# Kernel optimization log

Measured on AMD Instinct MI355X. Metric: run time of the kernel, lower is better.

## Reference

```python
import jax, jax.numpy as jnp
import numpy as np

B, S, D_IN, D_MID, D_OUT, V = 32, 512, 768, 128, 4, 100000
N = B * S  # static upper bound on number of unique (vocab_id, batch_id) pairs


def setup_inputs() -> dict:
    key = jax.random.key(0)
    k1, k2, k3, k4 = jax.random.split(key, 4)
    vocab_ids = jax.random.randint(k1, (B, S), 0, V)
    embeddings = jax.random.normal(k2, (B, S, D_IN), jnp.float32)
    # nn.Linear default init (kaiming-uniform-ish); exact distribution is irrelevant for correctness
    lin_bound = 1.0 / np.sqrt(D_IN)
    W1 = jax.random.uniform(k3, (D_IN, D_MID), jnp.float32, -lin_bound, lin_bound)
    b1 = jnp.zeros((D_MID,), jnp.float32)
    # kaiming_uniform_(a=sqrt(5)) on (V, D_MID, D_OUT): fan_in = D_MID*D_OUT, bound = 1/sqrt(fan_in)
    enc_bound = 1.0 / np.sqrt(D_MID * D_OUT)
    encoder_weights = jax.random.uniform(k4, (V, D_MID, D_OUT), jnp.float32, -enc_bound, enc_bound)
    return {"vocab_ids": vocab_ids, "embeddings": embeddings, "W1": W1, "b1": b1,
            "encoder_weights": encoder_weights}


def reference(vocab_ids, embeddings, W1, b1, encoder_weights):
    # Composite key = vocab_id * B + batch_id -> same lexicographic (vocab, batch) order
    # as torch.unique(dim=0) on stacked (vocab_id, batch_id) pairs.
    batch_ids = jnp.arange(B, dtype=vocab_ids.dtype)[:, None]            # (B,1)
    keys = (vocab_ids * B + batch_ids).reshape(-1)                        # (N,)
    # Static-size unique for jit; padded slots (fill) receive zero-sum embeddings.
    uniq_keys, inv = jnp.unique(keys, size=N, fill_value=0, return_inverse=True)
    flat_emb = embeddings.reshape(N, D_IN)
    summed = jax.ops.segment_sum(flat_emb, inv.reshape(-1), num_segments=N)  # (N, D_IN)
    h = jnp.tanh(summed @ W1 + b1)                                        # (N, D_MID)
    uniq_vocab = uniq_keys // B
    uniq_batch = uniq_keys % B
    Wtok = encoder_weights[uniq_vocab]                                    # (N, D_MID, D_OUT) gather
    encoded = jax.nn.sigmoid(jnp.einsum('bi,bio->bo', h, Wtok))           # (N, D_OUT)
    ids = jnp.stack([uniq_vocab, uniq_batch], axis=1)                     # (N, 2)
    return ids, encoded
```

## Files before the change

### kernel.cpp

```cpp
#include <hip/hip_runtime.h>
#include <hip/hip_bf16.h>

#define NELEM 16384
#define DIN 768
#define DMID 128
#define DOUT 4

typedef __attribute__((ext_vector_type(8))) short short8;
typedef __attribute__((ext_vector_type(4))) float f32x4;

__device__ __forceinline__ unsigned f2bf(float f) {
    unsigned u = __float_as_uint(f);
    return (u + 0x7FFFu + ((u >> 16) & 1u)) >> 16;
}


#define FAST_WS 557384
#define SORT_BLOCKS 64

__device__ __forceinline__ void gsync(unsigned* bar) {
    __syncthreads();
    if (threadIdx.x == 0) {
        unsigned g = __hip_atomic_load(&bar[1], __ATOMIC_ACQUIRE, __HIP_MEMORY_SCOPE_AGENT);
        unsigned a = __hip_atomic_fetch_add(&bar[0], 1u, __ATOMIC_ACQ_REL, __HIP_MEMORY_SCOPE_AGENT);
        if (a + 1u == (unsigned)SORT_BLOCKS) {
            __hip_atomic_store(&bar[0], 0u, __ATOMIC_RELAXED, __HIP_MEMORY_SCOPE_AGENT);
            __hip_atomic_store(&bar[1], g + 1u, __ATOMIC_RELEASE, __HIP_MEMORY_SCOPE_AGENT);
        } else {
            while (__hip_atomic_load(&bar[1], __ATOMIC_ACQUIRE, __HIP_MEMORY_SCOPE_AGENT) == g) {
                __builtin_amdgcn_s_sleep(2);
            }
        }
    }
    __syncthreads();
}

__global__ __launch_bounds__(256) void prep_kernel(
    const int* __restrict__ vocab_ids, const float* __restrict__ W1,
    unsigned* __restrict__ P0, unsigned* __restrict__ hist0,
    unsigned* __restrict__ histZ, unsigned short* __restrict__ WtG,
    unsigned* __restrict__ bar) {
    const int t = threadIdx.x;
    const int bx = blockIdx.x;
    if (bx < 64) {
        __shared__ unsigned h[256];
        h[t] = 0;
        int e = bx * 256 + t;
        unsigned word = ((unsigned)vocab_ids[e] << 14) | (unsigned)e;
        P0[e] = word;
        __syncthreads();
        atomicAdd(&h[(word >> 9) & 255u], 1u);
        __syncthreads();
        hist0[t * 64 + bx] = h[t];
        histZ[bx * 512 + t] = 0;
        histZ[bx * 512 + 256 + t] = 0;
        if (bx == 0 && t == 0) bar[0] = 0;
    } else {
        int idx = (bx - 64) * 256 + t;
        int c = idx / DIN;
        int k = idx - c * DIN;
        WtG[idx] = (unsigned short)f2bf(W1[k * DMID + c]);
    }
}

template <bool HASNEXT>
__device__ __forceinline__ void scatter_pass(
    const unsigned* __restrict__ src, unsigned* __restrict__ dst,
    const unsigned* __restrict__ histCur, unsigned* __restrict__ histNext,
    int shift, int nshift, int blk, int t,
    unsigned* base_lds, unsigned* whist, unsigned* wsum) {
    const int lane = t & 63;
    const int w = t >> 6;

    unsigned x = src[blk * 256 + t];
    unsigned d = (x >> shift) & 255u;

    whist[t] = 0; whist[256 + t] = 0; whist[512 + t] = 0; whist[768 + t] = 0;

    unsigned rowsum = 0, myprefix = 0;
    const uint4* row = (const uint4*)(histCur + t * 64);
#pragma unroll
    for (int q = 0; q < 16; ++q) {
        uint4 h4 = row[q];
        int b = q * 4;
        rowsum += h4.x + h4.y + h4.z + h4.w;
        if (b + 0 < blk) myprefix += h4.x;
        if (b + 1 < blk) myprefix += h4.y;
        if (b + 2 < blk) myprefix += h4.z;
        if (b + 3 < blk) myprefix += h4.w;
    }
    unsigned inc = rowsum;
#pragma unroll
    for (int off = 1; off < 64; off <<= 1) {
        unsigned y = __shfl_up(inc, off);
        if (lane >= off) inc += y;
    }
    if (lane == 63) wsum[w] = inc;
    __syncthreads();
    unsigned wo = 0;
    for (int w2 = 0; w2 < w; ++w2) wo += wsum[w2];
    base_lds[t] = wo + (inc - rowsum) + myprefix;

    unsigned long long m = ~0ull;
#pragma unroll
    for (int bit = 0; bit < 8; ++bit) {
        unsigned long long bb = __ballot((d >> bit) & 1u);
        m &= ((d >> bit) & 1u) ? bb : ~bb;
    }
    int inrank = __popcll(m & ((1ull << lane) - 1ull));
    if (inrank == 0) whist[w * 256 + d] = (unsigned)__popcll(m);
    __syncthreads();
    unsigned cross = 0;
    for (int w2 = 0; w2 < w; ++w2) cross += whist[w2 * 256 + d];
    unsigned dstpos = base_lds[d] + cross + (unsigned)inrank;
    dst[dstpos] = x;
    if (HASNEXT) {
        unsigned dn = (x >> nshift) & 255u;
        atomicAdd(&histNext[dn * 64 + (dstpos >> 8)], 1u);
    }
}

__global__ __launch_bounds__(256) void coop_sort_kernel(
    unsigned* __restrict__ P0, unsigned* __restrict__ P1,
    const unsigned* __restrict__ hist0, unsigned* __restrict__ hist1,
    unsigned* __restrict__ hist2,
    unsigned short* __restrict__ RS, float* __restrict__ out_ids,
    unsigned* __restrict__ bar) {
    __shared__ unsigned base_lds[256];
    __shared__ unsigned whist[4 * 256];
    __shared__ unsigned wsum[4];
    const int t = threadIdx.x;
    const int blk = blockIdx.x;
    unsigned* gsum = bar + 2;

    scatter_pass<true >(P0, P1, hist0, hist1, 9, 17, blk, t, base_lds, whist, wsum);
    gsync(bar);
    scatter_pass<true >(P1, P0, hist1, hist2, 17, 25, blk, t, base_lds, whist, wsum);
    gsync(bar);
    scatter_pass<false>(P0, P1, hist2, nullptr, 25, 0, blk, t, base_lds, whist, wsum);
    gsync(bar);

    const int e = blk * 256 + t;
    const int lane = t & 63;
    const int w = t >> 6;
    unsigned word = P1[e];
    unsigned key = word >> 9;
    bool f = (e == 0) || ((P1[e - 1] >> 9) != key);
    unsigned long long bb = __ballot(f ? 1 : 0);
    unsigned lrank = (unsigned)__popcll(bb & ((1ull << lane) - 1ull));
    if (lane == 0) wsum[w] = (unsigned)__popcll(bb);
    __syncthreads();
    unsigned woff = 0, btot = 0;
#pragma unroll
    for (int w2 = 0; w2 < 4; ++w2) {
        if (w2 < w) woff += wsum[w2];
        btot += wsum[w2];
    }
    if (t == 0) gsum[blk] = btot;
    gsync(bar);
    unsigned prefix = 0, U = 0;
#pragma unroll
    for (int b = 0; b < 64; ++b) {
        unsigned g = gsum[b];
        if (b < blk) prefix += g;
        U += g;
    }
    if (f) {
        unsigned r = prefix + woff + lrank;
        RS[r] = (unsigned short)e;
        out_ids[2 * r + 0] = (float)(word >> 14);
        out_ids[2 * r + 1] = (float)(key & 31u);
    }
    if ((unsigned)e >= U) {
        RS[e] = (unsigned short)NELEM;
        out_ids[2 * e + 0] = 0.0f;
        out_ids[2 * e + 1] = 0.0f;
    }
    if (e == 0) RS[NELEM] = (unsigned short)NELEM;
}

#define SORT_SMEM (65536 + 65536 + 4096 + 64)

__global__ __launch_bounds__(1024) void sort_transpose_kernel(
    const int* __restrict__ vocab_ids,
    const float* __restrict__ W1,
    unsigned int* __restrict__ G,
    unsigned short* __restrict__ RS,
    unsigned short* __restrict__ WtG,
    float* __restrict__ out_ids) {
    const int t = threadIdx.x;
    if (blockIdx.x != 0) {
        int idx = (blockIdx.x - 1) * 1024 + t;
        if (idx < DMID * DIN) {
            int c = idx / DIN;
            int k = idx - c * DIN;
            WtG[idx] = (unsigned short)f2bf(W1[k * DMID + c]);
        }
        return;
    }
    extern __shared__ char smem[];
    unsigned* Gs     = (unsigned*)smem;
    unsigned* histDM = (unsigned*)(smem + 65536);
    unsigned* sums   = (unsigned*)(smem + 131072);
    unsigned* totalU = (unsigned*)(smem + 135168);

    for (int e = t; e < NELEM; e += 1024)
        Gs[e] = ((unsigned)vocab_ids[e] << 14) | (unsigned)e;
    __syncthreads();

    for (int pass = 0; pass < 6; ++pass) {
        const int shift = 9 + pass * 4;
        unsigned v[16];
#pragma unroll
        for (int i = 0; i < 16; ++i) v[i] = Gs[t * 16 + i];
#pragma unroll
        for (int d = 0; d < 16; ++d) histDM[d * 1024 + t] = 0;
#pragma unroll
        for (int i = 0; i < 16; ++i) histDM[((v[i] >> shift) & 15u) * 1024 + t] += 1;
        __syncthreads();
        unsigned lex[16]; unsigned run = 0;
#pragma unroll
        for (int i = 0; i < 16; ++i) { unsigned x = histDM[t * 16 + i]; lex[i] = run; run += x; }
        sums[t] = run;
        __syncthreads();
        if (t < 64) {
            unsigned s[16]; unsigned tot = 0;
#pragma unroll
            for (int i = 0; i < 16; ++i) { unsigned x = sums[t * 16 + i]; s[i] = tot; tot += x; }
            unsigned incv = tot;
#pragma unroll
            for (int off = 1; off < 64; off <<= 1) {
                unsigned y = __shfl_up(incv, off);
                if (t >= off) incv += y;
            }
            unsigned excl = incv - tot;
#pragma unroll
            for (int i = 0; i < 16; ++i) sums[t * 16 + i] = excl + s[i];
        }
        __syncthreads();
#pragma unroll
        for (int i = 0; i < 16; ++i) histDM[t * 16 + i] = sums[t] + lex[i];
        __syncthreads();
        unsigned mycnt[16];
#pragma unroll
        for (int d = 0; d < 16; ++d) mycnt[d] = histDM[d * 1024 + t];
#pragma unroll
        for (int i = 0; i < 16; ++i) {
            unsigned d = (v[i] >> shift) & 15u;
            Gs[mycnt[d]++] = v[i];
        }
        __syncthreads();
    }

    unsigned v[16];
#pragma unroll
    for (int i = 0; i < 16; ++i) v[i] = Gs[t * 16 + i];
    unsigned pk = (t == 0) ? 0xFFFFFFFFu : (Gs[t * 16 - 1] >> 9);
    unsigned fm = 0;
#pragma unroll
    for (int i = 0; i < 16; ++i) {
        unsigned key = v[i] >> 9;
        if (key != pk) fm |= (1u << i);
        pk = key;
    }
    sums[t] = (unsigned)__popc(fm);
    __syncthreads();
    if (t < 64) {
        unsigned s[16]; unsigned tot = 0;
#pragma unroll
        for (int i = 0; i < 16; ++i) { unsigned x = sums[t * 16 + i]; s[i] = tot; tot += x; }
        unsigned incv = tot;
#pragma unroll
        for (int off = 1; off < 64; off <<= 1) {
            unsigned y = __shfl_up(incv, off);
            if (t >= off) incv += y;
        }
        unsigned excl = incv - tot;
#pragma unroll
        for (int i = 0; i < 16; ++i) sums[t * 16 + i] = excl + s[i];
        if (t == 63) *totalU = incv;
    }
    __syncthreads();
    unsigned r = sums[t];
#pragma unroll
    for (int i = 0; i < 16; ++i) {
        if (fm & (1u << i)) {
            RS[r] = (unsigned short)(t * 16 + i);
            out_ids[2 * r + 0] = (float)(v[i] >> 14);
            out_ids[2 * r + 1] = (float)((v[i] >> 9) & 31u);
            ++r;
        }
    }
    const unsigned U = *totalU;
    for (int u = t; u < NELEM; u += 1024) {
        if ((unsigned)u >= U) {
            RS[u] = (unsigned short)NELEM;
            out_ids[2 * u + 0] = 0.0f;
            out_ids[2 * u + 1] = 0.0f;
        }
        G[u] = Gs[u];
    }
    if (t == 0) RS[NELEM] = (unsigned short)NELEM;
}

#define FBM 16
__global__ __launch_bounds__(256) void fused_kernel(
    const unsigned* __restrict__ G,
    const unsigned short* __restrict__ RS,
    const unsigned short* __restrict__ WtG,
    const float* __restrict__ emb,
    const float* __restrict__ b1,
    const float* __restrict__ enc,
    float* __restrict__ out_enc) {
    __shared__ char smem[20736];

    const int t = threadIdx.x;
    const int u0 = blockIdx.x * FBM;
    const int l = t & 63;
    const int w = t >> 6;

    const int ar = t >> 4;
    const int ak4 = t & 15;
    const int rs_a = (int)RS[u0 + ar];
    const int re_a = (int)RS[u0 + ar + 1];

    f32x4 acc0 = {0.f, 0.f, 0.f, 0.f};
    f32x4 acc1 = {0.f, 0.f, 0.f, 0.f};

    for (int kk = 0; kk < DIN; kk += 64) {
        __syncthreads();
        {
            float s0 = 0.f, s1 = 0.f, s2 = 0.f, s3 = 0.f;
            const float* base = emb + (size_t)(kk + ak4 * 4);
            for (int p = rs_a; p < re_a; ++p) {
                unsigned idx = G[p] & 16383u;
                const float4 e4 = *(const float4*)(base + (size_t)idx * DIN);
                s0 += e4.x; s1 += e4.y; s2 += e4.z; s3 += e4.w;
            }
            uint2 packed;
            packed.x = f2bf(s0) | (f2bf(s1) << 16);
            packed.y = f2bf(s2) | (f2bf(s3) << 16);
            *(uint2*)(smem + ar * 144 + ak4 * 8) = packed;
        }
        {
#pragma unroll
            for (int i = 0; i < 4; ++i) {
                int q = t + i * 256;
                int c = q >> 3;
                int uo = q & 7;
                uint4 dv = *(const uint4*)(WtG + (size_t)c * DIN + kk + uo * 8);
                *(uint4*)(smem + 2304 + c * 144 + uo * 16) = dv;
            }
        }
        __syncthreads();
        {
            const int arow = l & 15;
            const int ull = l >> 4;
#pragma unroll
            for (int kf = 0; kf < 2; ++kf) {
                short8 aF = *(const short8*)(smem + arow * 144 + kf * 64 + ull * 16);
                short8 bF0 = *(const short8*)(smem + 2304 + (w * 32 + arow) * 144 + kf * 64 + ull * 16);
                short8 bF1 = *(const short8*)(smem + 2304 + (w * 32 + 16 + arow) * 144 + kf * 64 + ull * 16);
                acc0 = __builtin_amdgcn_mfma_f32_16x16x32_bf16(aF, bF0, acc0, 0, 0, 0);
                acc1 = __builtin_amdgcn_mfma_f32_16x16x32_bf16(aF, bF1, acc1, 0, 0, 0);
            }
        }
    }
    __syncthreads();
    {
        float* Hs = (float*)smem;
        const int col0 = w * 32 + (l & 15);
        const int rbase = (l >> 4) * 4;
#pragma unroll
        for (int reg = 0; reg < 4; ++reg) {
            Hs[(rbase + reg) * 132 + col0] = tanhf(acc0[reg] + b1[col0]);
            Hs[(rbase + reg) * 132 + col0 + 16] = tanhf(acc1[reg] + b1[col0 + 16]);
        }
    }
    __syncthreads();
    {
        const float* Hs = (const float*)smem;
        const int r = t >> 4;
        const int g = t & 15;
        const int u = u0 + r;
        const int rs = (int)RS[u];
        const int re = (int)RS[u + 1];
        unsigned vocab = (rs < re) ? (G[rs] >> 14) : 0u;
        const float4* wrow = (const float4*)(enc + (size_t)vocab * (DMID * DOUT));
        float ax = 0.f, ay = 0.f, az = 0.f, aw = 0.f;
#pragma unroll
        for (int jj = 0; jj < 8; ++jj) {
            int j = jj * 16 + g;
            float4 w4 = wrow[j];
            float hv = Hs[r * 132 + j];
            ax += hv * w4.x; ay += hv * w4.y; az += hv * w4.z; aw += hv * w4.w;
        }
#pragma unroll
        for (int off = 1; off < 16; off <<= 1) {
            ax += __shfl_xor(ax, off);
            ay += __shfl_xor(ay, off);
            az += __shfl_xor(az, off);
            aw += __shfl_xor(aw, off);
        }
        if (g == 0) {
            float4 o;
            o.x = 1.f / (1.f + expf(-ax));
            o.y = 1.f / (1.f + expf(-ay));
            o.z = 1.f / (1.f + expf(-az));
            o.w = 1.f / (1.f + expf(-aw));
            *(float4*)(out_enc + (size_t)u * 4) = o;
        }
    }
}

extern "C" void kernel_launch(void* const* d_in, const int* in_sizes, int n_in,
                              void* d_out, int out_size, void* d_ws, size_t ws_size,
                              hipStream_t stream) {
    const int*   vocab_ids = (const int*)d_in[0];
    const float* emb       = (const float*)d_in[1];
    const float* W1        = (const float*)d_in[2];
    const float* b1        = (const float*)d_in[3];
    const float* enc       = (const float*)d_in[4];
    float* out = (float*)d_out;

    float* out_ids = out;
    float* out_enc = out + NELEM * 2;

    char* ws = (char*)d_ws;

    if (ws_size >= FAST_WS) {
        unsigned*       P0    = (unsigned*)(ws + 0);
        unsigned*       P1    = (unsigned*)(ws + 65536);
        unsigned*       hist0 = (unsigned*)(ws + 131072);
        unsigned*       hist1 = (unsigned*)(ws + 196608);
        unsigned*       hist2 = (unsigned*)(ws + 262144);
        unsigned short* RS    = (unsigned short*)(ws + 327680);
        unsigned short* WtG   = (unsigned short*)(ws + 360512);
        unsigned*       bar   = (unsigned*)(ws + 557120);

        prep_kernel<<<448, 256, 0, stream>>>(vocab_ids, W1, P0, hist0, hist1, WtG, bar);
        coop_sort_kernel<<<SORT_BLOCKS, 256, 0, stream>>>(P0, P1, hist0, hist1, hist2,
                                                          RS, out_ids, bar);
        fused_kernel<<<NELEM / FBM, 256, 0, stream>>>(P1, RS, WtG, emb, b1, enc, out_enc);
    } else {
        unsigned int*   G   = (unsigned int*)(ws);
        unsigned short* RS  = (unsigned short*)(ws + 65536);
        unsigned short* WtG = (unsigned short*)(ws + 98432);

        hipFuncSetAttribute((const void*)sort_transpose_kernel,
                            hipFuncAttributeMaxDynamicSharedMemorySize, SORT_SMEM);
        sort_transpose_kernel<<<1 + 96, 1024, SORT_SMEM, stream>>>(
            vocab_ids, W1, G, RS, WtG, out_ids);
        fused_kernel<<<NELEM / FBM, 256, 0, stream>>>(G, RS, WtG, emb, b1, enc, out_enc);
    }
}
```

Before: 71.79 us.

## Fold prep into cooperative sort kernel with monotonic-counter grid barriers

Merges the histogram/transposition prep kernel into the persistent sort kernel, adding a grid barrier after prep. It replaces the generation-based barrier with a monotonically increasing counter reset by a memset each launch, and uses relaxed agent-scope atomics for cross-block data. Histogram layout is changed to block-major so each pass reads per-digit counts coalesced across threads. This removes one kernel launch but adds a memset, and the W1 transpose now runs on only 64 blocks.

```diff
diff --git a/kernel.cpp b/kernel.cpp
--- a/kernel.cpp
+++ b/kernel.cpp
@@ -15,52 +15,28 @@
 }
 
 
-#define FAST_WS 557384
-#define SORT_BLOCKS 64
-
-__device__ __forceinline__ void gsync(unsigned* bar) {
+#define FAST_WS 557440
+#define SB 64
+
+__device__ __forceinline__ unsigned aload(const unsigned* p) {
+    return __hip_atomic_load((unsigned*)p, __ATOMIC_RELAXED, __HIP_MEMORY_SCOPE_AGENT);
+}
+__device__ __forceinline__ void astore(unsigned* p, unsigned v) {
+    __hip_atomic_store(p, v, __ATOMIC_RELAXED, __HIP_MEMORY_SCOPE_AGENT);
+}
+__device__ __forceinline__ void aadd(unsigned* p, unsigned v) {
+    __hip_atomic_fetch_add(p, v, __ATOMIC_RELAXED, __HIP_MEMORY_SCOPE_AGENT);
+}
+
+__device__ __forceinline__ void gbar(unsigned* cnt, unsigned thresh) {
     __syncthreads();
     if (threadIdx.x == 0) {
-        unsigned g = __hip_atomic_load(&bar[1], __ATOMIC_ACQUIRE, __HIP_MEMORY_SCOPE_AGENT);
-        unsigned a = __hip_atomic_fetch_add(&bar[0], 1u, __ATOMIC_ACQ_REL, __HIP_MEMORY_SCOPE_AGENT);
-        if (a + 1u == (unsigned)SORT_BLOCKS) {
-            __hip_atomic_store(&bar[0], 0u, __ATOMIC_RELAXED, __HIP_MEMORY_SCOPE_AGENT);
-            __hip_atomic_store(&bar[1], g + 1u, __ATOMIC_RELEASE, __HIP_MEMORY_SCOPE_AGENT);
-        } else {
-            while (__hip_atomic_load(&bar[1], __ATOMIC_ACQUIRE, __HIP_MEMORY_SCOPE_AGENT) == g) {
-                __builtin_amdgcn_s_sleep(2);
-            }
-        }
-    }
-    __syncthreads();
-}
-
-__global__ __launch_bounds__(256) void prep_kernel(
-    const int* __restrict__ vocab_ids, const float* __restrict__ W1,
-    unsigned* __restrict__ P0, unsigned* __restrict__ hist0,
-    unsigned* __restrict__ histZ, unsigned short* __restrict__ WtG,
-    unsigned* __restrict__ bar) {
-    const int t = threadIdx.x;
-    const int bx = blockIdx.x;
-    if (bx < 64) {
-        __shared__ unsigned h[256];
-        h[t] = 0;
-        int e = bx * 256 + t;
-        unsigned word = ((unsigned)vocab_ids[e] << 14) | (unsigned)e;
-        P0[e] = word;
-        __syncthreads();
-        atomicAdd(&h[(word >> 9) & 255u], 1u);
-        __syncthreads();
-        hist0[t * 64 + bx] = h[t];
-        histZ[bx * 512 + t] = 0;
-        histZ[bx * 512 + 256 + t] = 0;
-        if (bx == 0 && t == 0) bar[0] = 0;
-    } else {
-        int idx = (bx - 64) * 256 + t;
-        int c = idx / DIN;
-        int k = idx - c * DIN;
-        WtG[idx] = (unsigned short)f2bf(W1[k * DMID + c]);
-    }
+        __hip_atomic_fetch_add(cnt, 1u, __ATOMIC_ACQ_REL, __HIP_MEMORY_SCOPE_AGENT);
+        while (__hip_atomic_load(cnt, __ATOMIC_RELAXED, __HIP_MEMORY_SCOPE_AGENT) < thresh)
+            __builtin_amdgcn_s_sleep(1);
+        (void)__hip_atomic_load(cnt, __ATOMIC_ACQUIRE, __HIP_MEMORY_SCOPE_AGENT);
+    }
+    __syncthreads();
 }
 
 template <bool HASNEXT>
@@ -72,22 +48,17 @@
     const int lane = t & 63;
     const int w = t >> 6;
 
-    unsigned x = src[blk * 256 + t];
+    unsigned x = aload(&src[blk * 256 + t]);
     unsigned d = (x >> shift) & 255u;
 
     whist[t] = 0; whist[256 + t] = 0; whist[512 + t] = 0; whist[768 + t] = 0;
 
     unsigned rowsum = 0, myprefix = 0;
-    const uint4* row = (const uint4*)(histCur + t * 64);
-#pragma unroll
-    for (int q = 0; q < 16; ++q) {
-        uint4 h4 = row[q];
-        int b = q * 4;
-        rowsum += h4.x + h4.y + h4.z + h4.w;
-        if (b + 0 < blk) myprefix += h4.x;
-        if (b + 1 < blk) myprefix += h4.y;
-        if (b + 2 < blk) myprefix += h4.z;
-        if (b + 3 < blk) myprefix += h4.w;
+#pragma unroll
+    for (int b = 0; b < SB; ++b) {
+        unsigned h = aload(&histCur[b * 256 + t]);
+        rowsum += h;
+        if (b < blk) myprefix += h;
     }
     unsigned inc = rowsum;
 #pragma unroll
@@ -113,70 +84,97 @@
     unsigned cross = 0;
     for (int w2 = 0; w2 < w; ++w2) cross += whist[w2 * 256 + d];
     unsigned dstpos = base_lds[d] + cross + (unsigned)inrank;
-    dst[dstpos] = x;
+    astore(&dst[dstpos], x);
     if (HASNEXT) {
         unsigned dn = (x >> nshift) & 255u;
-        atomicAdd(&histNext[dn * 64 + (dstpos >> 8)], 1u);
-    }
-}
-
-__global__ __launch_bounds__(256) void coop_sort_kernel(
+        aadd(&histNext[(dstpos >> 8) * 256 + dn], 1u);
+    }
+    __syncthreads();
+}
+
+__global__ __launch_bounds__(256) void sort_mega_kernel(
+    const int* __restrict__ vocab_ids, const float* __restrict__ W1,
     unsigned* __restrict__ P0, unsigned* __restrict__ P1,
-    const unsigned* __restrict__ hist0, unsigned* __restrict__ hist1,
+    unsigned* __restrict__ hist0, unsigned* __restrict__ hist1,
     unsigned* __restrict__ hist2,
-    unsigned short* __restrict__ RS, float* __restrict__ out_ids,
-    unsigned* __restrict__ bar) {
+    unsigned short* __restrict__ RS, unsigned short* __restrict__ WtG,
+    float* __restrict__ out_ids,
+    unsigned* __restrict__ bar, unsigned* __restrict__ gsum) {
     __shared__ unsigned base_lds[256];
     __shared__ unsigned whist[4 * 256];
     __shared__ unsigned wsum[4];
     const int t = threadIdx.x;
     const int blk = blockIdx.x;
-    unsigned* gsum = bar + 2;
+
+    const int e = blk * 256 + t;
+    {
+        whist[t] = 0;
+        unsigned word = ((unsigned)vocab_ids[e] << 14) | (unsigned)e;
+        astore(&P0[e], word);
+        __syncthreads();
+        atomicAdd(&whist[(word >> 9) & 255u], 1u);
+        __syncthreads();
+        astore(&hist0[blk * 256 + t], whist[t]);
+        astore(&hist1[blk * 256 + t], 0u);
+        astore(&hist2[blk * 256 + t], 0u);
+#pragma unroll
+        for (int i = 0; i < 6; ++i) {
+            int j = blk * 1536 + i * 256 + t;
+            int k = j >> 7;
+            int c = j & 127;
+            WtG[c * DIN + k] = (unsigned short)f2bf(W1[j]);
+        }
+        __syncthreads();
+    }
+    gbar(bar, SB * 1);
 
     scatter_pass<true >(P0, P1, hist0, hist1, 9, 17, blk, t, base_lds, whist, wsum);
-    gsync(bar);
+    gbar(bar, SB * 2);
     scatter_pass<true >(P1, P0, hist1, hist2, 17, 25, blk, t, base_lds, whist, wsum);
-    gsync(bar);
+    gbar(bar, SB * 3);
     scatter_pass<false>(P0, P1, hist2, nullptr, 25, 0, blk, t, base_lds, whist, wsum);
-    gsync(bar);
-
-    const int e = blk * 256 + t;
-    const int lane = t & 63;
-    const int w = t >> 6;
-    unsigned word = P1[e];
+    gbar(bar, SB * 4);
+
+    unsigned word = aload(&P1[e]);
     unsigned key = word >> 9;
-    bool f = (e == 0) || ((P1[e - 1] >> 9) != key);
-    unsigned long long bb = __ballot(f ? 1 : 0);
-    unsigned lrank = (unsigned)__popcll(bb & ((1ull << lane) - 1ull));
-    if (lane == 0) wsum[w] = (unsigned)__popcll(bb);
-    __syncthreads();
-    unsigned woff = 0, btot = 0;
-#pragma unroll
-    for (int w2 = 0; w2 < 4; ++w2) {
-        if (w2 < w) woff += wsum[w2];
-        btot += wsum[w2];
-    }
-    if (t == 0) gsum[blk] = btot;
-    gsync(bar);
-    unsigned prefix = 0, U = 0;
-#pragma unroll
-    for (int b = 0; b < 64; ++b) {
-        unsigned g = gsum[b];
-        if (b < blk) prefix += g;
-        U += g;
-    }
-    if (f) {
-        unsigned r = prefix + woff + lrank;
-        RS[r] = (unsigned short)e;
-        out_ids[2 * r + 0] = (float)(word >> 14);
-        out_ids[2 * r + 1] = (float)(key & 31u);
-    }
-    if ((unsigned)e >= U) {
-        RS[e] = (unsigned short)NELEM;
-        out_ids[2 * e + 0] = 0.0f;
-        out_ids[2 * e + 1] = 0.0f;
-    }
-    if (e == 0) RS[NELEM] = (unsigned short)NELEM;
+    bool f = (e == 0) || ((aload(&P1[e - 1]) >> 9) != key);
+    {
+        const int lane = t & 63;
+        const int w = t >> 6;
+        unsigned long long bb = __ballot(f ? 1 : 0);
+        unsigned lrank = (unsigned)__popcll(bb & ((1ull << lane) - 1ull));
+        if (lane == 0) wsum[w] = (unsigned)__popcll(bb);
+        __syncthreads();
+        unsigned woff = 0, btot = 0;
+#pragma unroll
+        for (int w2 = 0; w2 < 4; ++w2) {
+            if (w2 < w) woff += wsum[w2];
+            btot += wsum[w2];
+        }
+        if (t == 0) astore(&gsum[blk], btot);
+        gbar(bar, SB * 5);
+        if (t < SB) base_lds[t] = aload(&gsum[t]);
+        __syncthreads();
+        unsigned prefix = 0, U = 0;
+#pragma unroll
+        for (int b = 0; b < SB; ++b) {
+            unsigned g = base_lds[b];
+            if (b < blk) prefix += g;
+            U += g;
+        }
+        if (f) {
+            unsigned r = prefix + woff + lrank;
+            RS[r] = (unsigned short)e;
+            out_ids[2 * r + 0] = (float)(word >> 14);
+            out_ids[2 * r + 1] = (float)(key & 31u);
+        }
+        if ((unsigned)e >= U) {
+            RS[e] = (unsigned short)NELEM;
+            out_ids[2 * e + 0] = 0.0f;
+            out_ids[2 * e + 1] = 0.0f;
+        }
+        if (e == 0) RS[NELEM] = (unsigned short)NELEM;
+    }
 }
 
 #define SORT_SMEM (65536 + 65536 + 4096 + 64)
@@ -437,10 +435,12 @@
         unsigned short* RS    = (unsigned short*)(ws + 327680);
         unsigned short* WtG   = (unsigned short*)(ws + 360512);
         unsigned*       bar   = (unsigned*)(ws + 557120);
-
-        prep_kernel<<<448, 256, 0, stream>>>(vocab_ids, W1, P0, hist0, hist1, WtG, bar);
-        coop_sort_kernel<<<SORT_BLOCKS, 256, 0, stream>>>(P0, P1, hist0, hist1, hist2,
-                                                          RS, out_ids, bar);
+        unsigned*       gsum  = (unsigned*)(ws + 557184);
+
+        hipMemsetAsync(bar, 0, 4, stream);
+        sort_mega_kernel<<<SB, 256, 0, stream>>>(vocab_ids, W1, P0, P1,
+                                                 hist0, hist1, hist2,
+                                                 RS, WtG, out_ids, bar, gsum);
         fused_kernel<<<NELEM / FBM, 256, 0, stream>>>(P1, RS, WtG, emb, b1, enc, out_enc);
     } else {
         unsigned int*   G   = (unsigned int*)(ws);
```

New measurement: 66.91 us. 1.07x faster.
